# Kernel tuning notes

Hardware: AMD Instinct MI355X
Metric: run time of the kernel (lower is better)

Reference implementation:

```python
import jax, jax.numpy as jnp
import numpy as np

N = 200000   # gaussians
M = 10000    # scaffold nodes
K = 16       # skinning knn
T = 40       # time steps
F = 32       # semantic feature dim
MAX_S = 0.1
MIN_S = 0.0
EPS = 1e-8


def _qnorm(q):
    return q / jnp.clip(jnp.linalg.norm(q, axis=-1, keepdims=True), 1e-12)


def q2R(q):
    # quaternion (w, x, y, z) -> rotation matrix, normalizing first (matches q2R in source)
    q = _qnorm(q)
    w, x, y, z = q[..., 0], q[..., 1], q[..., 2], q[..., 3]
    r0 = jnp.stack([1 - 2 * (y * y + z * z), 2 * (x * y - w * z), 2 * (x * z + w * y)], -1)
    r1 = jnp.stack([2 * (x * y + w * z), 1 - 2 * (x * x + z * z), 2 * (y * z - w * x)], -1)
    r2 = jnp.stack([2 * (x * z - w * y), 2 * (y * z + w * x), 1 - 2 * (x * x + y * y)], -1)
    return jnp.stack([r0, r1, r2], -2)


def quat_mul(a, b):
    aw, ax, ay, az = a[..., 0], a[..., 1], a[..., 2], a[..., 3]
    bw, bx, by, bz = b[..., 0], b[..., 1], b[..., 2], b[..., 3]
    return jnp.stack([
        aw * bw - ax * bx - ay * by - az * bz,
        aw * bx + ax * bw + ay * bz - az * by,
        aw * by - ax * bz + ay * bw + az * bx,
        aw * bz + ax * by - ay * bx + az * bw], -1)


def quat_conj(q):
    return q * jnp.array([1.0, -1.0, -1.0, -1.0], q.dtype)


def setup_inputs() -> dict:
    key = jax.random.key(0)
    ks = jax.random.split(key, 13)
    return {
        "gs_xyz": 0.05 * jax.random.normal(ks[0], (N, 3), jnp.float32),
        "gs_rotation": jax.random.normal(ks[1], (N, 4), jnp.float32),
        "gs_scaling": jax.random.normal(ks[2], (N, 3), jnp.float32),
        "gs_opacity": jax.random.normal(ks[3], (N, 1), jnp.float32),
        "feat_dc": jax.random.normal(ks[4], (N, 3), jnp.float32),
        "feat_rest": jax.random.normal(ks[5], (N, 9), jnp.float32),
        "node_xyz": jax.random.normal(ks[6], (T, M, 3), jnp.float32),
        "node_quat": jax.random.normal(ks[7], (T, M, 4), jnp.float32),
        "node_sigma": 0.1 + 0.5 * jax.random.uniform(ks[8], (M, 1), jnp.float32),
        "node_sem": jax.random.normal(ks[9], (M, F), jnp.float32),
        "attach_ind": jax.random.randint(ks[10], (N,), 0, M, jnp.int32),
        "ref_time": jax.random.randint(ks[11], (N,), 0, T, jnp.int32),
        "topo_knn": jax.random.randint(ks[12], (M, K), 0, M, jnp.int32),
        "t": 5,
    }


def reference(gs_xyz, gs_rotation, gs_scaling, gs_opacity, feat_dc, feat_rest,
              node_xyz, node_quat, node_sigma, node_sem,
              attach_ind, ref_time, topo_knn, t):
    # --- per-gaussian activated attributes ---
    s = MIN_S + jax.nn.sigmoid(gs_scaling) * (MAX_S - MIN_S)   # s_act
    o = jax.nn.sigmoid(gs_opacity)                              # o_act
    sph = jnp.concatenate([feat_dc, feat_rest], axis=-1)        # [N, 12], full sph order

    # --- leaf-local -> world at ref time (get_xyz / get_R_mtx) ---
    ref_p_attach = node_xyz[ref_time, attach_ind]               # [N,3] async knn gather
    ref_q_attach = node_quat[ref_time, attach_ind]              # [N,4]
    R_ref_attach = q2R(ref_q_attach)                            # [N,3,3]
    x_world = jnp.einsum('nij,nj->ni', R_ref_attach, gs_xyz) + ref_p_attach
    R_world = jnp.einsum('nij,njk->nik', R_ref_attach, q2R(gs_rotation))

    # --- scf.warp: KNN skinning from per-point ref time to target time t ---
    sk_ind = topo_knn[attach_ind]                               # [N,K] neighbor node ids
    p_ref = node_xyz[ref_time[:, None], sk_ind]                 # [N,K,3]
    q_ref = node_quat[ref_time[:, None], sk_ind]                # [N,K,4]
    p_live = node_xyz[t][sk_ind]                                # [N,K,3]
    q_live = node_quat[t][sk_ind]                               # [N,K,4]
    sigma = node_sigma[sk_ind, 0]                               # [N,K]

    diff = x_world[:, None, :] - p_ref                          # [N,K,3]
    dsq = jnp.sum(diff * diff, axis=-1)                         # [N,K]
    w = jnp.exp(-dsq / (2.0 * sigma * sigma + EPS))             # RBF skinning weights
    w = w / (jnp.sum(w, axis=-1, keepdims=True) + EPS)          # [N,K]

    # per-node relative transform ref -> live
    q_rel = quat_mul(_qnorm(q_live), quat_conj(_qnorm(q_ref)))  # [N,K,4]
    R_rel = q2R(q_rel)                                          # [N,K,3,3]
    mu_k = jnp.einsum('nkij,nkj->nki', R_rel, diff) + p_live    # [N,K,3]
    mu_live = jnp.einsum('nk,nki->ni', w, mu_k)                 # [N,3]

    q_blend = jnp.einsum('nk,nkd->nd', w, q_rel)                # blended quaternion
    fr_live = jnp.einsum('nij,njk->nik', q2R(q_blend), R_world) # [N,3,3]

    sem_live = jnp.einsum('nk,nkf->nf', w, node_sem[sk_ind])    # [N,F]

    return mu_live, fr_live, s, o, sph, sem_live
```

## Files before the change

kernel.cpp:

```cpp
#include <hip/hip_runtime.h>

#define KNN 16
#define FSEM 32
#define LPG 4
#define NXCD 8
#define NSUB 256

__device__ __forceinline__ float sigmoidf_(float x) { return 1.0f / (1.0f + __expf(-x)); }

__device__ __forceinline__ void quat_to_R(float qw, float qx, float qy, float qz, float* R) {
    float d = qw * qw + qx * qx + qy * qy + qz * qz;
    float inv = rsqrtf(fmaxf(d, 1e-24f));
    float w = qw * inv, x = qx * inv, y = qy * inv, z = qz * inv;
    R[0] = 1.f - 2.f * (y * y + z * z); R[1] = 2.f * (x * y - w * z); R[2] = 2.f * (x * z + w * y);
    R[3] = 2.f * (x * y + w * z); R[4] = 1.f - 2.f * (x * x + z * z); R[5] = 2.f * (y * z - w * x);
    R[6] = 2.f * (x * z - w * y); R[7] = 2.f * (y * z + w * x); R[8] = 1.f - 2.f * (x * x + y * y);
}

__global__ void __launch_bounds__(256)
k_pack_hist(const float* __restrict__ node_xyz, const float* __restrict__ node_quat,
            const float* __restrict__ node_sigma,
            const int* __restrict__ attach, const int* __restrict__ rtime,
            float* __restrict__ packed, int* __restrict__ cnt, int* __restrict__ rank,
            int TM, int M, int N, int shift)
{
    int p = blockIdx.x * blockDim.x + threadIdx.x;
    if (p < TM) {
        const int node = p - (p / M) * M;
        const float* x = node_xyz + 3 * (size_t)p;
        float4 a = make_float4(x[0], x[1], x[2], node_sigma[node]);
        float4 q = reinterpret_cast<const float4*>(node_quat)[p];
        float4* dst = reinterpret_cast<float4*>(packed + 8 * (size_t)p);
        dst[0] = a;
        dst[1] = q;
    }
    if (p < N && cnt) {
        const int key = rtime[p] * NSUB + (attach[p] >> shift);
        rank[p] = atomicAdd(&cnt[key], 1);
    }
}

__global__ void __launch_bounds__(256)
k_scan1(int* __restrict__ cnt, int* __restrict__ blk, int B)
{
    __shared__ int sh[256];
    const int i = blockIdx.x * 256 + threadIdx.x;
    int v = (i < B) ? cnt[i] : 0;
    sh[threadIdx.x] = v;
    __syncthreads();
    int acc = v;
#pragma unroll
    for (int off = 1; off < 256; off <<= 1) {
        int u = (threadIdx.x >= off) ? sh[threadIdx.x - off] : 0;
        __syncthreads();
        acc += u;
        sh[threadIdx.x] = acc;
        __syncthreads();
    }
    if (i < B) cnt[i] = acc - v;
    if (threadIdx.x == 255) blk[blockIdx.x] = acc;
}

__global__ void __launch_bounds__(256)
k_scan2(int* __restrict__ blk, int nblk)
{
    __shared__ int sh[256];
    __shared__ int carry_s;
    if (threadIdx.x == 0) carry_s = 0;
    __syncthreads();
    for (int base = 0; base < nblk; base += 256) {
        const int i = base + threadIdx.x;
        int v = (i < nblk) ? blk[i] : 0;
        sh[threadIdx.x] = v;
        __syncthreads();
        int acc = v;
#pragma unroll
        for (int off = 1; off < 256; off <<= 1) {
            int u = (threadIdx.x >= off) ? sh[threadIdx.x - off] : 0;
            __syncthreads();
            acc += u;
            sh[threadIdx.x] = acc;
            __syncthreads();
        }
        const int carry = carry_s;
        if (i < nblk) blk[i] = acc - v + carry;
        __syncthreads();
        if (threadIdx.x == 255) carry_s = carry + acc;
        __syncthreads();
    }
}

__global__ void __launch_bounds__(256)
k_scatter_elem(const int* __restrict__ attach, const int* __restrict__ rtime,
               const float* __restrict__ gs_xyz,
               const int* __restrict__ rank, const int* __restrict__ cnt,
               const int* __restrict__ blk,
               float4* __restrict__ meta,
               const float* __restrict__ gs_scal,
               const float* __restrict__ gs_opa,
               const float* __restrict__ feat_dc,
               const float* __restrict__ feat_rest,
               float* __restrict__ out,
               int N, int shift)
{
    int n = blockIdx.x * blockDim.x + threadIdx.x;
    if (n >= N) return;
    const int a = attach[n], rt = rtime[n];
    const int key = rt * NSUB + (a >> shift);
    const int pos = cnt[key] + blk[key >> 8] + rank[n];
    meta[2 * (size_t)pos]     = make_float4(__int_as_float(n), __int_as_float(a),
                                            __int_as_float(rt), 0.f);
    meta[2 * (size_t)pos + 1] = make_float4(gs_xyz[3 * (size_t)n + 0],
                                            gs_xyz[3 * (size_t)n + 1],
                                            gs_xyz[3 * (size_t)n + 2], 0.f);

    const size_t Ns = (size_t)N, ns = (size_t)n;
    float* os = out + 12 * Ns + 3 * ns;
    os[0] = 0.1f * sigmoidf_(gs_scal[3 * ns + 0]);
    os[1] = 0.1f * sigmoidf_(gs_scal[3 * ns + 1]);
    os[2] = 0.1f * sigmoidf_(gs_scal[3 * ns + 2]);

    out[15 * Ns + ns] = sigmoidf_(gs_opa[ns]);

    float* osph = out + 16 * Ns + 12 * ns;
    float4 v0 = make_float4(feat_dc[3 * ns + 0], feat_dc[3 * ns + 1], feat_dc[3 * ns + 2],
                            feat_rest[9 * ns + 0]);
    float4 v1 = make_float4(feat_rest[9 * ns + 1], feat_rest[9 * ns + 2],
                            feat_rest[9 * ns + 3], feat_rest[9 * ns + 4]);
    float4 v2 = make_float4(feat_rest[9 * ns + 5], feat_rest[9 * ns + 6],
                            feat_rest[9 * ns + 7], feat_rest[9 * ns + 8]);
    reinterpret_cast<float4*>(osph)[0] = v0;
    reinterpret_cast<float4*>(osph)[1] = v1;
    reinterpret_cast<float4*>(osph)[2] = v2;
}

__global__ void __launch_bounds__(256)
k_elem(const float* __restrict__ gs_scal,
       const float* __restrict__ gs_opa,
       const float* __restrict__ feat_dc,
       const float* __restrict__ feat_rest,
       float* __restrict__ out, int N)
{
    const int n = blockIdx.x * blockDim.x + threadIdx.x;
    if (n >= N) return;
    const size_t Ns = (size_t)N, ns = (size_t)n;

    float* os = out + 12 * Ns + 3 * ns;
    os[0] = 0.1f * sigmoidf_(gs_scal[3 * ns + 0]);
    os[1] = 0.1f * sigmoidf_(gs_scal[3 * ns + 1]);
    os[2] = 0.1f * sigmoidf_(gs_scal[3 * ns + 2]);

    out[15 * Ns + ns] = sigmoidf_(gs_opa[ns]);

    float* osph = out + 16 * Ns + 12 * ns;
    float4 v0 = make_float4(feat_dc[3 * ns + 0], feat_dc[3 * ns + 1], feat_dc[3 * ns + 2],
                            feat_rest[9 * ns + 0]);
    float4 v1 = make_float4(feat_rest[9 * ns + 1], feat_rest[9 * ns + 2],
                            feat_rest[9 * ns + 3], feat_rest[9 * ns + 4]);
    float4 v2 = make_float4(feat_rest[9 * ns + 5], feat_rest[9 * ns + 6],
                            feat_rest[9 * ns + 7], feat_rest[9 * ns + 8]);
    reinterpret_cast<float4*>(osph)[0] = v0;
    reinterpret_cast<float4*>(osph)[1] = v1;
    reinterpret_cast<float4*>(osph)[2] = v2;
}

template<bool PACKED, bool SORTED>
__global__ void __launch_bounds__(256)
dynscf_kernel(const float* __restrict__ gs_xyz,
              const float* __restrict__ gs_rot,
              const float* __restrict__ node_xyz,
              const float* __restrict__ node_quat,
              const float* __restrict__ packed,
              const float* __restrict__ node_sigma,
              const float* __restrict__ node_sem,
              const int* __restrict__ attach_ind,
              const int* __restrict__ ref_time,
              const int* __restrict__ topo_knn,
              const int* __restrict__ t_ptr,
              const float4* __restrict__ meta,
              float* __restrict__ out,
              int N, int M)
{
    int bid = blockIdx.x;
    if (SORTED) {
        const int nwg = gridDim.x;
        const int q = nwg / NXCD, r = nwg % NXCD;
        const int xcd = bid % NXCD, idx = bid / NXCD;
        bid = (xcd < r ? xcd * (q + 1) : r * (q + 1) + (xcd - r) * q) + idx;
    }
    const int tid = bid * blockDim.x + threadIdx.x;
    const int g   = tid >> 2;
    const int sub = tid & (LPG - 1);
    if (g >= N) return;

    const int t = t_ptr[0];

    int n, a, rt;
    float gx, gy, gz;
    if (SORTED) {
        const float4 m0 = meta[2 * (size_t)g];
        const float4 m1 = meta[2 * (size_t)g + 1];
        n  = __float_as_int(m0.x);
        a  = __float_as_int(m0.y);
        rt = __float_as_int(m0.z);
        gx = m1.x; gy = m1.y; gz = m1.z;
    } else {
        n  = g;
        a  = attach_ind[n];
        rt = ref_time[n];
        gx = gs_xyz[3 * (size_t)n + 0];
        gy = gs_xyz[3 * (size_t)n + 1];
        gz = gs_xyz[3 * (size_t)n + 2];
    }

    const size_t base_rt = (size_t)rt * (size_t)M;
    const size_t base_t  = (size_t)t  * (size_t)M;

    const int4 kv = reinterpret_cast<const int4*>(topo_knn)[(size_t)a * (KNN / 4) + sub];
    const int js[4] = { kv.x, kv.y, kv.z, kv.w };

    float apx, apy, apz, aqw, aqx, aqy, aqz;
    if (PACKED) {
        const float4* pk = reinterpret_cast<const float4*>(packed + (base_rt + (size_t)a) * 8);
        float4 xz = pk[0], qv = pk[1];
        apx = xz.x; apy = xz.y; apz = xz.z;
        aqw = qv.x; aqx = qv.y; aqy = qv.z; aqz = qv.w;
    } else {
        const float4 qv = *reinterpret_cast<const float4*>(node_quat + (base_rt + (size_t)a) * 4);
        const float* pa = node_xyz + (base_rt + (size_t)a) * 3;
        apx = pa[0]; apy = pa[1]; apz = pa[2];
        aqw = qv.x; aqx = qv.y; aqy = qv.z; aqz = qv.w;
    }
    float Rref[9];
    quat_to_R(aqw, aqx, aqy, aqz, Rref);

    const float xw0 = Rref[0] * gx + Rref[1] * gy + Rref[2] * gz + apx;
    const float xw1 = Rref[3] * gx + Rref[4] * gy + Rref[5] * gz + apy;
    const float xw2 = Rref[6] * gx + Rref[7] * gy + Rref[8] * gz + apz;

    float wsum = 0.f, mu0 = 0.f, mu1 = 0.f, mu2 = 0.f;
    float qb0 = 0.f, qb1 = 0.f, qb2 = 0.f, qb3 = 0.f;
    float wk[4];

#pragma unroll
    for (int k = 0; k < KNN / LPG; k++) {
        const int j = js[k];

        float prx, pry, prz, rw, rx, ry, rz;
        float plx, ply, plz, lw, lx, ly, lz;
        float sg;
        if (PACKED) {
            const float4* pkr = reinterpret_cast<const float4*>(packed + (base_rt + (size_t)j) * 8);
            float4 xr = pkr[0], qr = pkr[1];
            prx = xr.x; pry = xr.y; prz = xr.z; sg = xr.w;
            rw = qr.x; rx = qr.y; ry = qr.z; rz = qr.w;
            const float4* pkl = reinterpret_cast<const float4*>(packed + (base_t + (size_t)j) * 8);
            float4 xl = pkl[0], ql = pkl[1];
            plx = xl.x; ply = xl.y; plz = xl.z;
            lw = ql.x; lx = ql.y; ly = ql.z; lz = ql.w;
        } else {
            const float* pr = node_xyz + (base_rt + (size_t)j) * 3;
            prx = pr[0]; pry = pr[1]; prz = pr[2];
            const float4 qr = *reinterpret_cast<const float4*>(node_quat + (base_rt + (size_t)j) * 4);
            rw = qr.x; rx = qr.y; ry = qr.z; rz = qr.w;
            const float* pl = node_xyz + (base_t + (size_t)j) * 3;
            plx = pl[0]; ply = pl[1]; plz = pl[2];
            const float4 ql = *reinterpret_cast<const float4*>(node_quat + (base_t + (size_t)j) * 4);
            lw = ql.x; lx = ql.y; ly = ql.z; lz = ql.w;
            sg = node_sigma[j];
        }

        const float dx = xw0 - prx;
        const float dy = xw1 - pry;
        const float dz = xw2 - prz;
        const float dsq = dx * dx + dy * dy + dz * dz;

        const float w = __expf(-dsq / (2.f * sg * sg + 1e-8f));
        wk[k] = w;

        {
            float inv = rsqrtf(fmaxf(rw * rw + rx * rx + ry * ry + rz * rz, 1e-24f));
            rw *= inv; rx *= inv; ry *= inv; rz *= inv;
        }
        {
            float inv = rsqrtf(fmaxf(lw * lw + lx * lx + ly * ly + lz * lz, 1e-24f));
            lw *= inv; lx *= inv; ly *= inv; lz *= inv;
        }
        const float qw =  lw * rw + lx * rx + ly * ry + lz * rz;
        const float qx = -lw * rx + lx * rw - ly * rz + lz * ry;
        const float qy = -lw * ry + lx * rz + ly * rw - lz * rx;
        const float qz = -lw * rz - lx * ry + ly * rx + lz * rw;

        float Rr[9];
        quat_to_R(qw, qx, qy, qz, Rr);

        const float m0 = Rr[0] * dx + Rr[1] * dy + Rr[2] * dz + plx;
        const float m1 = Rr[3] * dx + Rr[4] * dy + Rr[5] * dz + ply;
        const float m2 = Rr[6] * dx + Rr[7] * dy + Rr[8] * dz + plz;

        wsum += w;
        mu0 += w * m0; mu1 += w * m1; mu2 += w * m2;
        qb0 += w * qw; qb1 += w * qx; qb2 += w * qy; qb3 += w * qz;
    }

#pragma unroll
    for (int m = 1; m < LPG; m <<= 1) {
        wsum += __shfl_xor(wsum, m);
        mu0  += __shfl_xor(mu0, m);  mu1 += __shfl_xor(mu1, m);  mu2 += __shfl_xor(mu2, m);
        qb0  += __shfl_xor(qb0, m);  qb1 += __shfl_xor(qb1, m);
        qb2  += __shfl_xor(qb2, m);  qb3 += __shfl_xor(qb3, m);
    }

    const float invw = 1.f / (wsum + 1e-8f);
    const size_t Ns = (size_t)N, ns = (size_t)n;

    float sm0 = 0.f, sm1 = 0.f, sm2 = 0.f, sm3 = 0.f;
    float sm4 = 0.f, sm5 = 0.f, sm6 = 0.f, sm7 = 0.f;
    const float4* sem4 = reinterpret_cast<const float4*>(node_sem);
#pragma unroll
    for (int kk = 0; kk < KNN; kk++) {
        const int src = kk >> 2;
        const int idx = kk & 3;
        const int   jk = __shfl(js[idx], src, LPG);
        const float wkk = __shfl(wk[idx], src, LPG);
        const float4 v0 = sem4[(size_t)jk * (FSEM / 4) + sub * 2 + 0];
        const float4 v1 = sem4[(size_t)jk * (FSEM / 4) + sub * 2 + 1];
        sm0 += wkk * v0.x; sm1 += wkk * v0.y; sm2 += wkk * v0.z; sm3 += wkk * v0.w;
        sm4 += wkk * v1.x; sm5 += wkk * v1.y; sm6 += wkk * v1.z; sm7 += wkk * v1.w;
    }

    if (sub == 0) {
        out[3 * ns + 0] = mu0 * invw;
        out[3 * ns + 1] = mu1 * invw;
        out[3 * ns + 2] = mu2 * invw;
    } else if (sub == 1) {
        const float4 qg = *reinterpret_cast<const float4*>(gs_rot + 4 * ns);
        float Rg[9];
        quat_to_R(qg.x, qg.y, qg.z, qg.w, Rg);
        float Rw[9];
#pragma unroll
        for (int i = 0; i < 3; i++)
#pragma unroll
            for (int j = 0; j < 3; j++)
                Rw[3 * i + j] = Rref[3 * i] * Rg[j] + Rref[3 * i + 1] * Rg[3 + j] + Rref[3 * i + 2] * Rg[6 + j];
        float Rb[9];
        quat_to_R(qb0 * invw, qb1 * invw, qb2 * invw, qb3 * invw, Rb);
        float* ofr = out + 3 * Ns + 9 * ns;
#pragma unroll
        for (int i = 0; i < 3; i++)
#pragma unroll
            for (int j = 0; j < 3; j++)
                ofr[3 * i + j] = Rb[3 * i] * Rw[j] + Rb[3 * i + 1] * Rw[3 + j] + Rb[3 * i + 2] * Rw[6 + j];
    }

    float4* osem = reinterpret_cast<float4*>(out + 28 * Ns + FSEM * ns);
    osem[sub * 2 + 0] = make_float4(sm0 * invw, sm1 * invw, sm2 * invw, sm3 * invw);
    osem[sub * 2 + 1] = make_float4(sm4 * invw, sm5 * invw, sm6 * invw, sm7 * invw);
}

extern "C" void kernel_launch(void* const* d_in, const int* in_sizes, int n_in,
                              void* d_out, int out_size, void* d_ws, size_t ws_size,
                              hipStream_t stream)
{
    const float* gs_xyz     = (const float*)d_in[0];
    const float* gs_rot     = (const float*)d_in[1];
    const float* gs_scal    = (const float*)d_in[2];
    const float* gs_opa     = (const float*)d_in[3];
    const float* feat_dc    = (const float*)d_in[4];
    const float* feat_rest  = (const float*)d_in[5];
    const float* node_xyz   = (const float*)d_in[6];
    const float* node_quat  = (const float*)d_in[7];
    const float* node_sigma = (const float*)d_in[8];
    const float* node_sem   = (const float*)d_in[9];
    const int* attach_ind   = (const int*)d_in[10];
    const int* ref_time     = (const int*)d_in[11];
    const int* topo_knn     = (const int*)d_in[12];
    const int* t_ptr        = (const int*)d_in[13];

    const int N = in_sizes[0] / 3;
    const int M = in_sizes[8];
    const int TM = in_sizes[6] / 3;
    const int T  = TM / M;
    const int B  = T * NSUB;

    int shift = 0;
    while (((M - 1) >> shift) >= NSUB) shift++;

    float* out = (float*)d_out;

    const int block = 256;
    const int gridN = (N + block - 1) / block;
    const long long threads = (long long)N * LPG;
    const int gridM = (int)((threads + block - 1) / block);
    const int gridPH = (((TM > N ? TM : N)) + block - 1) / block;
    const int nblkS = (B + 255) / 256;

    const size_t f_packed = (size_t)TM * 8;
    const size_t f_meta   = (size_t)N * 8;
    const size_t i_cnt    = (size_t)B;
    const size_t i_blk    = (size_t)nblkS;
    const size_t i_rank   = (size_t)N;
    const size_t need_sort   = (f_packed + f_meta + i_cnt + i_blk + i_rank) * sizeof(float);
    const size_t need_packed = f_packed * sizeof(float);

    if (ws_size >= need_sort) {
        float*  packed = (float*)d_ws;
        float4* meta   = (float4*)(packed + f_packed);
        int*    cnt    = (int*)(packed + f_packed + f_meta);
        int*    blk    = cnt + i_cnt;
        int*    rank   = blk + i_blk;

        hipMemsetAsync(cnt, 0, (size_t)B * sizeof(int), stream);
        hipLaunchKernelGGL(k_pack_hist, dim3(gridPH), dim3(block), 0, stream,
                           node_xyz, node_quat, node_sigma, attach_ind, ref_time,
                           packed, cnt, rank, TM, M, N, shift);
        hipLaunchKernelGGL(k_scan1, dim3(nblkS), dim3(block), 0, stream, cnt, blk, B);
        hipLaunchKernelGGL(k_scan2, dim3(1), dim3(block), 0, stream, blk, nblkS);
        hipLaunchKernelGGL(k_scatter_elem, dim3(gridN), dim3(block), 0, stream,
                           attach_ind, ref_time, gs_xyz, rank, cnt, blk, meta,
                           gs_scal, gs_opa, feat_dc, feat_rest, out, N, shift);
        hipLaunchKernelGGL((dynscf_kernel<true, true>), dim3(gridM), dim3(block), 0, stream,
                           gs_xyz, gs_rot, node_xyz, node_quat, packed, node_sigma, node_sem,
                           attach_ind, ref_time, topo_knn, t_ptr, meta, out, N, M);
    } else if (ws_size >= need_packed) {
        float* packed = (float*)d_ws;
        hipLaunchKernelGGL(k_pack_hist, dim3(gridPH), dim3(block), 0, stream,
                           node_xyz, node_quat, node_sigma, attach_ind, ref_time,
                           packed, (int*)nullptr, (int*)nullptr, TM, M, 0, shift);
        hipLaunchKernelGGL((dynscf_kernel<true, false>), dim3(gridM), dim3(block), 0, stream,
                           gs_xyz, gs_rot, node_xyz, node_quat, packed, node_sigma, node_sem,
                           attach_ind, ref_time, topo_knn, t_ptr, (const float4*)nullptr,
                           out, N, M);
        hipLaunchKernelGGL(k_elem, dim3(gridN), dim3(block), 0, stream,
                           gs_scal, gs_opa, feat_dc, feat_rest, out, N);
    } else {
        hipLaunchKernelGGL((dynscf_kernel<false, false>), dim3(gridM), dim3(block), 0, stream,
                           gs_xyz, gs_rot, node_xyz, node_quat, (const float*)nullptr,
                           node_sigma, node_sem,
                           attach_ind, ref_time, topo_knn, t_ptr, (const float4*)nullptr,
                           out, N, M);
        hipLaunchKernelGGL(k_elem, dim3(gridN), dim3(block), 0, stream,
                           gs_scal, gs_opa, feat_dc, feat_rest, out, N);
    }
}
```

Baseline: 216.3 us.

## Replace two-level counting sort with per-timestep block-aggregated bucket sort

Drops the fine key (ref_time × attach bucket) counting sort and its two scan kernels. Instead it bins only by ref_time, using shared-memory histograms with one global atomic per block per timestep, and computes each block's offset with a serial prefix over T. It also packs the gaussian rotation into the sorted meta record so the main kernel reads it contiguously, and moves the reference rotation matrix into the sub==1 lane to shorten live ranges. The aim is fewer launches and less contention on global atomics. The cost is coarser sorting: elements are no longer grouped by attach node, so gather locality within a timestep may drop, and the meta record grows by one float4 per gaussian.

```diff
diff --git a/kernel.cpp b/kernel.cpp
--- a/kernel.cpp
+++ b/kernel.cpp
@@ -4,7 +4,8 @@
 #define FSEM 32
 #define LPG 4
 #define NXCD 8
-#define NSUB 256
+#define CSTRIDE 32
+#define MAXT 256
 
 __device__ __forceinline__ float sigmoidf_(float x) { return 1.0f / (1.0f + __expf(-x)); }
 
@@ -20,11 +21,17 @@
 __global__ void __launch_bounds__(256)
 k_pack_hist(const float* __restrict__ node_xyz, const float* __restrict__ node_quat,
             const float* __restrict__ node_sigma,
-            const int* __restrict__ attach, const int* __restrict__ rtime,
-            float* __restrict__ packed, int* __restrict__ cnt, int* __restrict__ rank,
-            int TM, int M, int N, int shift)
+            const int* __restrict__ rtime,
+            float* __restrict__ packed, int* __restrict__ cnt,
+            int TM, int M, int N, int T)
 {
-    int p = blockIdx.x * blockDim.x + threadIdx.x;
+    __shared__ int lh[MAXT];
+    if (threadIdx.x < MAXT) lh[threadIdx.x] = 0;
+    __syncthreads();
+
+    const int p = blockIdx.x * blockDim.x + threadIdx.x;
+    if (cnt && p < N) atomicAdd(&lh[rtime[p]], 1);
+
     if (p < TM) {
         const int node = p - (p / M) * M;
         const float* x = node_xyz + 3 * (size_t)p;
@@ -34,85 +41,66 @@
         dst[0] = a;
         dst[1] = q;
     }
-    if (p < N && cnt) {
-        const int key = rtime[p] * NSUB + (attach[p] >> shift);
-        rank[p] = atomicAdd(&cnt[key], 1);
-    }
-}
-
-__global__ void __launch_bounds__(256)
-k_scan1(int* __restrict__ cnt, int* __restrict__ blk, int B)
-{
-    __shared__ int sh[256];
-    const int i = blockIdx.x * 256 + threadIdx.x;
-    int v = (i < B) ? cnt[i] : 0;
-    sh[threadIdx.x] = v;
-    __syncthreads();
-    int acc = v;
-#pragma unroll
-    for (int off = 1; off < 256; off <<= 1) {
-        int u = (threadIdx.x >= off) ? sh[threadIdx.x - off] : 0;
-        __syncthreads();
-        acc += u;
-        sh[threadIdx.x] = acc;
-        __syncthreads();
-    }
-    if (i < B) cnt[i] = acc - v;
-    if (threadIdx.x == 255) blk[blockIdx.x] = acc;
-}
-
-__global__ void __launch_bounds__(256)
-k_scan2(int* __restrict__ blk, int nblk)
-{
-    __shared__ int sh[256];
-    __shared__ int carry_s;
-    if (threadIdx.x == 0) carry_s = 0;
-    __syncthreads();
-    for (int base = 0; base < nblk; base += 256) {
-        const int i = base + threadIdx.x;
-        int v = (i < nblk) ? blk[i] : 0;
-        sh[threadIdx.x] = v;
-        __syncthreads();
-        int acc = v;
-#pragma unroll
-        for (int off = 1; off < 256; off <<= 1) {
-            int u = (threadIdx.x >= off) ? sh[threadIdx.x - off] : 0;
-            __syncthreads();
-            acc += u;
-            sh[threadIdx.x] = acc;
-            __syncthreads();
-        }
-        const int carry = carry_s;
-        if (i < nblk) blk[i] = acc - v + carry;
-        __syncthreads();
-        if (threadIdx.x == 255) carry_s = carry + acc;
-        __syncthreads();
+
+    __syncthreads();
+    if (cnt && threadIdx.x < T) {
+        const int c = lh[threadIdx.x];
+        if (c > 0) atomicAdd(&cnt[threadIdx.x * CSTRIDE], c);
     }
 }
 
 __global__ void __launch_bounds__(256)
 k_scatter_elem(const int* __restrict__ attach, const int* __restrict__ rtime,
                const float* __restrict__ gs_xyz,
-               const int* __restrict__ rank, const int* __restrict__ cnt,
-               const int* __restrict__ blk,
+               const float* __restrict__ gs_rot,
+               const int* __restrict__ cnt, int* __restrict__ cur,
                float4* __restrict__ meta,
                const float* __restrict__ gs_scal,
                const float* __restrict__ gs_opa,
                const float* __restrict__ feat_dc,
                const float* __restrict__ feat_rest,
                float* __restrict__ out,
-               int N, int shift)
+               int N, int T)
 {
-    int n = blockIdx.x * blockDim.x + threadIdx.x;
-    if (n >= N) return;
-    const int a = attach[n], rt = rtime[n];
-    const int key = rt * NSUB + (a >> shift);
-    const int pos = cnt[key] + blk[key >> 8] + rank[n];
-    meta[2 * (size_t)pos]     = make_float4(__int_as_float(n), __int_as_float(a),
-                                            __int_as_float(rt), 0.f);
-    meta[2 * (size_t)pos + 1] = make_float4(gs_xyz[3 * (size_t)n + 0],
+    __shared__ int lh[MAXT];
+    __shared__ int bb[MAXT];
+    __shared__ int pref[MAXT];
+
+    if (threadIdx.x < MAXT) lh[threadIdx.x] = 0;
+    __syncthreads();
+
+    const int n = blockIdx.x * blockDim.x + threadIdx.x;
+    const bool valid = (n < N);
+    int a = 0, rt = 0, lrank = 0;
+    if (valid) {
+        a  = attach[n];
+        rt = rtime[n];
+        lrank = atomicAdd(&lh[rt], 1);
+    }
+    __syncthreads();
+
+    if (threadIdx.x < T) {
+        const int c = lh[threadIdx.x];
+        bb[threadIdx.x] = (c > 0) ? atomicAdd(&cur[threadIdx.x * CSTRIDE], c) : 0;
+        pref[threadIdx.x] = cnt[threadIdx.x * CSTRIDE];
+    }
+    __syncthreads();
+    if (threadIdx.x == 0) {
+        int run = 0;
+#pragma unroll 4
+        for (int i = 0; i < T; i++) { const int c = pref[i]; pref[i] = run; run += c; }
+    }
+    __syncthreads();
+
+    if (!valid) return;
+
+    const int pos = pref[rt] + bb[rt] + lrank;
+    meta[3 * (size_t)pos]     = make_float4(__int_as_float(n), 0.f,
+                                            __int_as_float(rt), __int_as_float(a));
+    meta[3 * (size_t)pos + 1] = make_float4(gs_xyz[3 * (size_t)n + 0],
                                             gs_xyz[3 * (size_t)n + 1],
                                             gs_xyz[3 * (size_t)n + 2], 0.f);
+    meta[3 * (size_t)pos + 2] = reinterpret_cast<const float4*>(gs_rot)[n];
 
     const size_t Ns = (size_t)N, ns = (size_t)n;
     float* os = out + 12 * Ns + 3 * ns;
@@ -198,11 +186,11 @@
     int n, a, rt;
     float gx, gy, gz;
     if (SORTED) {
-        const float4 m0 = meta[2 * (size_t)g];
-        const float4 m1 = meta[2 * (size_t)g + 1];
+        const float4 m0 = meta[3 * (size_t)g];
+        const float4 m1 = meta[3 * (size_t)g + 1];
         n  = __float_as_int(m0.x);
-        a  = __float_as_int(m0.y);
         rt = __float_as_int(m0.z);
+        a  = __float_as_int(m0.w);
         gx = m1.x; gy = m1.y; gz = m1.z;
     } else {
         n  = g;
@@ -231,12 +219,14 @@
         apx = pa[0]; apy = pa[1]; apz = pa[2];
         aqw = qv.x; aqx = qv.y; aqy = qv.z; aqz = qv.w;
     }
-    float Rref[9];
-    quat_to_R(aqw, aqx, aqy, aqz, Rref);
-
-    const float xw0 = Rref[0] * gx + Rref[1] * gy + Rref[2] * gz + apx;
-    const float xw1 = Rref[3] * gx + Rref[4] * gy + Rref[5] * gz + apy;
-    const float xw2 = Rref[6] * gx + Rref[7] * gy + Rref[8] * gz + apz;
+    float xw0, xw1, xw2;
+    {
+        float Rf[9];
+        quat_to_R(aqw, aqx, aqy, aqz, Rf);
+        xw0 = Rf[0] * gx + Rf[1] * gy + Rf[2] * gz + apx;
+        xw1 = Rf[3] * gx + Rf[4] * gy + Rf[5] * gz + apy;
+        xw2 = Rf[6] * gx + Rf[7] * gy + Rf[8] * gz + apz;
+    }
 
     float wsum = 0.f, mu0 = 0.f, mu1 = 0.f, mu2 = 0.f;
     float qb0 = 0.f, qb1 = 0.f, qb2 = 0.f, qb3 = 0.f;
@@ -334,7 +324,11 @@
         out[3 * ns + 1] = mu1 * invw;
         out[3 * ns + 2] = mu2 * invw;
     } else if (sub == 1) {
-        const float4 qg = *reinterpret_cast<const float4*>(gs_rot + 4 * ns);
+        float4 qg;
+        if (SORTED) qg = meta[3 * (size_t)g + 2];
+        else        qg = *reinterpret_cast<const float4*>(gs_rot + 4 * ns);
+        float Rref[9];
+        quat_to_R(aqw, aqx, aqy, aqz, Rref);
         float Rg[9];
         quat_to_R(qg.x, qg.y, qg.z, qg.w, Rg);
         float Rw[9];
@@ -381,10 +375,6 @@
     const int M = in_sizes[8];
     const int TM = in_sizes[6] / 3;
     const int T  = TM / M;
-    const int B  = T * NSUB;
-
-    int shift = 0;
-    while (((M - 1) >> shift) >= NSUB) shift++;
 
     float* out = (float*)d_out;
 
@@ -393,40 +383,35 @@
     const long long threads = (long long)N * LPG;
     const int gridM = (int)((threads + block - 1) / block);
     const int gridPH = (((TM > N ? TM : N)) + block - 1) / block;
-    const int nblkS = (B + 255) / 256;
 
     const size_t f_packed = (size_t)TM * 8;
-    const size_t f_meta   = (size_t)N * 8;
-    const size_t i_cnt    = (size_t)B;
-    const size_t i_blk    = (size_t)nblkS;
-    const size_t i_rank   = (size_t)N;
-    const size_t need_sort   = (f_packed + f_meta + i_cnt + i_blk + i_rank) * sizeof(float);
+    const size_t f_meta   = (size_t)N * 12;
+    const size_t i_cnt    = (size_t)MAXT * CSTRIDE;
+    const size_t i_cur    = (size_t)MAXT * CSTRIDE;
+    const size_t need_sort   = (f_packed + f_meta + i_cnt + i_cur) * sizeof(float);
     const size_t need_packed = f_packed * sizeof(float);
 
-    if (ws_size >= need_sort) {
+    if (ws_size >= need_sort && T <= MAXT) {
         float*  packed = (float*)d_ws;
         float4* meta   = (float4*)(packed + f_packed);
         int*    cnt    = (int*)(packed + f_packed + f_meta);
-        int*    blk    = cnt + i_cnt;
-        int*    rank   = blk + i_blk;
-
-        hipMemsetAsync(cnt, 0, (size_t)B * sizeof(int), stream);
+        int*    cur    = cnt + i_cnt;
+
+        hipMemsetAsync(cnt, 0, (i_cnt + i_cur) * sizeof(int), stream);
         hipLaunchKernelGGL(k_pack_hist, dim3(gridPH), dim3(block), 0, stream,
-                           node_xyz, node_quat, node_sigma, attach_ind, ref_time,
-                           packed, cnt, rank, TM, M, N, shift);
-        hipLaunchKernelGGL(k_scan1, dim3(nblkS), dim3(block), 0, stream, cnt, blk, B);
-        hipLaunchKernelGGL(k_scan2, dim3(1), dim3(block), 0, stream, blk, nblkS);
+                           node_xyz, node_quat, node_sigma, ref_time,
+                           packed, cnt, TM, M, N, T);
         hipLaunchKernelGGL(k_scatter_elem, dim3(gridN), dim3(block), 0, stream,
-                           attach_ind, ref_time, gs_xyz, rank, cnt, blk, meta,
-                           gs_scal, gs_opa, feat_dc, feat_rest, out, N, shift);
+                           attach_ind, ref_time, gs_xyz, gs_rot, cnt, cur, meta,
+                           gs_scal, gs_opa, feat_dc, feat_rest, out, N, T);
         hipLaunchKernelGGL((dynscf_kernel<true, true>), dim3(gridM), dim3(block), 0, stream,
                            gs_xyz, gs_rot, node_xyz, node_quat, packed, node_sigma, node_sem,
                            attach_ind, ref_time, topo_knn, t_ptr, meta, out, N, M);
     } else if (ws_size >= need_packed) {
         float* packed = (float*)d_ws;
         hipLaunchKernelGGL(k_pack_hist, dim3(gridPH), dim3(block), 0, stream,
-                           node_xyz, node_quat, node_sigma, attach_ind, ref_time,
-                           packed, (int*)nullptr, (int*)nullptr, TM, M, 0, shift);
+                           node_xyz, node_quat, node_sigma, ref_time,
+                           packed, (int*)nullptr, TM, M, 0, T);
         hipLaunchKernelGGL((dynscf_kernel<true, false>), dim3(gridM), dim3(block), 0, stream,
                            gs_xyz, gs_rot, node_xyz, node_quat, packed, node_sigma, node_sem,
                            attach_ind, ref_time, topo_knn, t_ptr, (const float4*)nullptr,
```

Result: no change. 212.2 us (-1.9%).

## Sort gaussians by exact (time,node) key, prenormalize node quats, gather rotations

Applied to the files above, without the earlier changes.

Replaces the coarse 256-bucket sort with a full counting sort keyed on (ref_time, attach node), so the rank array goes away and positions come from atomics during the scatter. Node quaternions are normalized once in the pack kernel, which removes the per-neighbor rsqrt work in the main kernel. Gaussian rotations are also scattered into sorted order so the main kernel reads them contiguously. The costs are a larger histogram and scan (T*M entries instead of T*256), more bytes written during the scatter, and within-bucket order that now depends on atomic ordering.

```diff
diff --git a/kernel.cpp b/kernel.cpp
--- a/kernel.cpp
+++ b/kernel.cpp
@@ -4,7 +4,6 @@
 #define FSEM 32
 #define LPG 4
 #define NXCD 8
-#define NSUB 256
 
 __device__ __forceinline__ float sigmoidf_(float x) { return 1.0f / (1.0f + __expf(-x)); }
 
@@ -17,26 +16,54 @@
     R[6] = 2.f * (x * z - w * y); R[7] = 2.f * (y * z + w * x); R[8] = 1.f - 2.f * (x * x + y * y);
 }
 
+__device__ __forceinline__ void elem_outputs(int n, int N,
+                                             const float* __restrict__ gs_scal,
+                                             const float* __restrict__ gs_opa,
+                                             const float* __restrict__ feat_dc,
+                                             const float* __restrict__ feat_rest,
+                                             float* __restrict__ out)
+{
+    const size_t Ns = (size_t)N, ns = (size_t)n;
+    float* os = out + 12 * Ns + 3 * ns;
+    os[0] = 0.1f * sigmoidf_(gs_scal[3 * ns + 0]);
+    os[1] = 0.1f * sigmoidf_(gs_scal[3 * ns + 1]);
+    os[2] = 0.1f * sigmoidf_(gs_scal[3 * ns + 2]);
+
+    out[15 * Ns + ns] = sigmoidf_(gs_opa[ns]);
+
+    float* osph = out + 16 * Ns + 12 * ns;
+    float4 v0 = make_float4(feat_dc[3 * ns + 0], feat_dc[3 * ns + 1], feat_dc[3 * ns + 2],
+                            feat_rest[9 * ns + 0]);
+    float4 v1 = make_float4(feat_rest[9 * ns + 1], feat_rest[9 * ns + 2],
+                            feat_rest[9 * ns + 3], feat_rest[9 * ns + 4]);
+    float4 v2 = make_float4(feat_rest[9 * ns + 5], feat_rest[9 * ns + 6],
+                            feat_rest[9 * ns + 7], feat_rest[9 * ns + 8]);
+    reinterpret_cast<float4*>(osph)[0] = v0;
+    reinterpret_cast<float4*>(osph)[1] = v1;
+    reinterpret_cast<float4*>(osph)[2] = v2;
+}
+
 __global__ void __launch_bounds__(256)
 k_pack_hist(const float* __restrict__ node_xyz, const float* __restrict__ node_quat,
             const float* __restrict__ node_sigma,
             const int* __restrict__ attach, const int* __restrict__ rtime,
-            float* __restrict__ packed, int* __restrict__ cnt, int* __restrict__ rank,
-            int TM, int M, int N, int shift)
-{
-    int p = blockIdx.x * blockDim.x + threadIdx.x;
+            float* __restrict__ packed, int* __restrict__ cnt,
+            int TM, int M, int N)
+{
+    const int p = blockIdx.x * blockDim.x + threadIdx.x;
     if (p < TM) {
         const int node = p - (p / M) * M;
         const float* x = node_xyz + 3 * (size_t)p;
+        float4 q = reinterpret_cast<const float4*>(node_quat)[p];
+        const float inv = rsqrtf(fmaxf(q.x * q.x + q.y * q.y + q.z * q.z + q.w * q.w, 1e-24f));
+        q.x *= inv; q.y *= inv; q.z *= inv; q.w *= inv;
         float4 a = make_float4(x[0], x[1], x[2], node_sigma[node]);
-        float4 q = reinterpret_cast<const float4*>(node_quat)[p];
         float4* dst = reinterpret_cast<float4*>(packed + 8 * (size_t)p);
         dst[0] = a;
         dst[1] = q;
     }
-    if (p < N && cnt) {
-        const int key = rtime[p] * NSUB + (attach[p] >> shift);
-        rank[p] = atomicAdd(&cnt[key], 1);
+    if (cnt && p < N) {
+        atomicAdd(&cnt[rtime[p] * M + attach[p]], 1);
     }
 }
 
@@ -93,45 +120,30 @@
 __global__ void __launch_bounds__(256)
 k_scatter_elem(const int* __restrict__ attach, const int* __restrict__ rtime,
                const float* __restrict__ gs_xyz,
-               const int* __restrict__ rank, const int* __restrict__ cnt,
-               const int* __restrict__ blk,
-               float4* __restrict__ meta,
+               const float* __restrict__ gs_rot,
+               int* __restrict__ cnt, const int* __restrict__ blk,
+               float4* __restrict__ metaA, float4* __restrict__ rotA,
                const float* __restrict__ gs_scal,
                const float* __restrict__ gs_opa,
                const float* __restrict__ feat_dc,
                const float* __restrict__ feat_rest,
                float* __restrict__ out,
-               int N, int shift)
-{
-    int n = blockIdx.x * blockDim.x + threadIdx.x;
+               int N, int M)
+{
+    const int n = blockIdx.x * blockDim.x + threadIdx.x;
     if (n >= N) return;
     const int a = attach[n], rt = rtime[n];
-    const int key = rt * NSUB + (a >> shift);
-    const int pos = cnt[key] + blk[key >> 8] + rank[n];
-    meta[2 * (size_t)pos]     = make_float4(__int_as_float(n), __int_as_float(a),
-                                            __int_as_float(rt), 0.f);
-    meta[2 * (size_t)pos + 1] = make_float4(gs_xyz[3 * (size_t)n + 0],
-                                            gs_xyz[3 * (size_t)n + 1],
-                                            gs_xyz[3 * (size_t)n + 2], 0.f);
-
-    const size_t Ns = (size_t)N, ns = (size_t)n;
-    float* os = out + 12 * Ns + 3 * ns;
-    os[0] = 0.1f * sigmoidf_(gs_scal[3 * ns + 0]);
-    os[1] = 0.1f * sigmoidf_(gs_scal[3 * ns + 1]);
-    os[2] = 0.1f * sigmoidf_(gs_scal[3 * ns + 2]);
-
-    out[15 * Ns + ns] = sigmoidf_(gs_opa[ns]);
-
-    float* osph = out + 16 * Ns + 12 * ns;
-    float4 v0 = make_float4(feat_dc[3 * ns + 0], feat_dc[3 * ns + 1], feat_dc[3 * ns + 2],
-                            feat_rest[9 * ns + 0]);
-    float4 v1 = make_float4(feat_rest[9 * ns + 1], feat_rest[9 * ns + 2],
-                            feat_rest[9 * ns + 3], feat_rest[9 * ns + 4]);
-    float4 v2 = make_float4(feat_rest[9 * ns + 5], feat_rest[9 * ns + 6],
-                            feat_rest[9 * ns + 7], feat_rest[9 * ns + 8]);
-    reinterpret_cast<float4*>(osph)[0] = v0;
-    reinterpret_cast<float4*>(osph)[1] = v1;
-    reinterpret_cast<float4*>(osph)[2] = v2;
+    const int key = rt * M + a;
+    const int pos = blk[key >> 8] + atomicAdd(&cnt[key], 1);
+
+    metaA[2 * (size_t)pos]     = make_float4(__int_as_float(n), __int_as_float(a),
+                                             __int_as_float(rt), 0.f);
+    metaA[2 * (size_t)pos + 1] = make_float4(gs_xyz[3 * (size_t)n + 0],
+                                             gs_xyz[3 * (size_t)n + 1],
+                                             gs_xyz[3 * (size_t)n + 2], 0.f);
+    rotA[pos] = reinterpret_cast<const float4*>(gs_rot)[n];
+
+    elem_outputs(n, N, gs_scal, gs_opa, feat_dc, feat_rest, out);
 }
 
 __global__ void __launch_bounds__(256)
@@ -143,25 +155,7 @@
 {
     const int n = blockIdx.x * blockDim.x + threadIdx.x;
     if (n >= N) return;
-    const size_t Ns = (size_t)N, ns = (size_t)n;
-
-    float* os = out + 12 * Ns + 3 * ns;
-    os[0] = 0.1f * sigmoidf_(gs_scal[3 * ns + 0]);
-    os[1] = 0.1f * sigmoidf_(gs_scal[3 * ns + 1]);
-    os[2] = 0.1f * sigmoidf_(gs_scal[3 * ns + 2]);
-
-    out[15 * Ns + ns] = sigmoidf_(gs_opa[ns]);
-
-    float* osph = out + 16 * Ns + 12 * ns;
-    float4 v0 = make_float4(feat_dc[3 * ns + 0], feat_dc[3 * ns + 1], feat_dc[3 * ns + 2],
-                            feat_rest[9 * ns + 0]);
-    float4 v1 = make_float4(feat_rest[9 * ns + 1], feat_rest[9 * ns + 2],
-                            feat_rest[9 * ns + 3], feat_rest[9 * ns + 4]);
-    float4 v2 = make_float4(feat_rest[9 * ns + 5], feat_rest[9 * ns + 6],
-                            feat_rest[9 * ns + 7], feat_rest[9 * ns + 8]);
-    reinterpret_cast<float4*>(osph)[0] = v0;
-    reinterpret_cast<float4*>(osph)[1] = v1;
-    reinterpret_cast<float4*>(osph)[2] = v2;
+    elem_outputs(n, N, gs_scal, gs_opa, feat_dc, feat_rest, out);
 }
 
 template<bool PACKED, bool SORTED>
@@ -177,7 +171,8 @@
               const int* __restrict__ ref_time,
               const int* __restrict__ topo_knn,
               const int* __restrict__ t_ptr,
-              const float4* __restrict__ meta,
+              const float4* __restrict__ metaA,
+              const float4* __restrict__ rotA,
               float* __restrict__ out,
               int N, int M)
 {
@@ -198,8 +193,8 @@
     int n, a, rt;
     float gx, gy, gz;
     if (SORTED) {
-        const float4 m0 = meta[2 * (size_t)g];
-        const float4 m1 = meta[2 * (size_t)g + 1];
+        const float4 m0 = metaA[2 * (size_t)g];
+        const float4 m1 = metaA[2 * (size_t)g + 1];
         n  = __float_as_int(m0.x);
         a  = __float_as_int(m0.y);
         rt = __float_as_int(m0.z);
@@ -231,12 +226,14 @@
         apx = pa[0]; apy = pa[1]; apz = pa[2];
         aqw = qv.x; aqx = qv.y; aqy = qv.z; aqz = qv.w;
     }
-    float Rref[9];
-    quat_to_R(aqw, aqx, aqy, aqz, Rref);
-
-    const float xw0 = Rref[0] * gx + Rref[1] * gy + Rref[2] * gz + apx;
-    const float xw1 = Rref[3] * gx + Rref[4] * gy + Rref[5] * gz + apy;
-    const float xw2 = Rref[6] * gx + Rref[7] * gy + Rref[8] * gz + apz;
+    float xw0, xw1, xw2;
+    {
+        float Rf[9];
+        quat_to_R(aqw, aqx, aqy, aqz, Rf);
+        xw0 = Rf[0] * gx + Rf[1] * gy + Rf[2] * gz + apx;
+        xw1 = Rf[3] * gx + Rf[4] * gy + Rf[5] * gz + apy;
+        xw2 = Rf[6] * gx + Rf[7] * gy + Rf[8] * gz + apz;
+    }
 
     float wsum = 0.f, mu0 = 0.f, mu1 = 0.f, mu2 = 0.f;
     float qb0 = 0.f, qb1 = 0.f, qb2 = 0.f, qb3 = 0.f;
@@ -278,12 +275,10 @@
         const float w = __expf(-dsq / (2.f * sg * sg + 1e-8f));
         wk[k] = w;
 
-        {
+        if (!PACKED) {
             float inv = rsqrtf(fmaxf(rw * rw + rx * rx + ry * ry + rz * rz, 1e-24f));
             rw *= inv; rx *= inv; ry *= inv; rz *= inv;
-        }
-        {
-            float inv = rsqrtf(fmaxf(lw * lw + lx * lx + ly * ly + lz * lz, 1e-24f));
+            inv = rsqrtf(fmaxf(lw * lw + lx * lx + ly * ly + lz * lz, 1e-24f));
             lw *= inv; lx *= inv; ly *= inv; lz *= inv;
         }
         const float qw =  lw * rw + lx * rx + ly * ry + lz * rz;
@@ -334,7 +329,11 @@
         out[3 * ns + 1] = mu1 * invw;
         out[3 * ns + 2] = mu2 * invw;
     } else if (sub == 1) {
-        const float4 qg = *reinterpret_cast<const float4*>(gs_rot + 4 * ns);
+        float4 qg;
+        if (SORTED) qg = rotA[g];
+        else        qg = *reinterpret_cast<const float4*>(gs_rot + 4 * ns);
+        float Rref[9];
+        quat_to_R(aqw, aqx, aqy, aqz, Rref);
         float Rg[9];
         quat_to_R(qg.x, qg.y, qg.z, qg.w, Rg);
         float Rw[9];
@@ -380,11 +379,8 @@
     const int N = in_sizes[0] / 3;
     const int M = in_sizes[8];
     const int TM = in_sizes[6] / 3;
-    const int T  = TM / M;
-    const int B  = T * NSUB;
-
-    int shift = 0;
-    while (((M - 1) >> shift) >= NSUB) shift++;
+    const int B  = TM;
+    const int nchunk = (B + 255) / 256;
 
     float* out = (float*)d_out;
 
@@ -393,52 +389,52 @@
     const long long threads = (long long)N * LPG;
     const int gridM = (int)((threads + block - 1) / block);
     const int gridPH = (((TM > N ? TM : N)) + block - 1) / block;
-    const int nblkS = (B + 255) / 256;
 
     const size_t f_packed = (size_t)TM * 8;
     const size_t f_meta   = (size_t)N * 8;
+    const size_t f_rot    = (size_t)N * 4;
     const size_t i_cnt    = (size_t)B;
-    const size_t i_blk    = (size_t)nblkS;
-    const size_t i_rank   = (size_t)N;
-    const size_t need_sort   = (f_packed + f_meta + i_cnt + i_blk + i_rank) * sizeof(float);
+    const size_t i_blk    = 4096;
+    const size_t need_sort   = (f_packed + f_meta + f_rot + i_cnt + i_blk) * sizeof(float);
     const size_t need_packed = f_packed * sizeof(float);
 
-    if (ws_size >= need_sort) {
+    if (ws_size >= need_sort && nchunk <= 4096) {
         float*  packed = (float*)d_ws;
-        float4* meta   = (float4*)(packed + f_packed);
-        int*    cnt    = (int*)(packed + f_packed + f_meta);
+        float4* metaA  = (float4*)(packed + f_packed);
+        float4* rotA   = (float4*)(packed + f_packed + f_meta);
+        int*    cnt    = (int*)(packed + f_packed + f_meta + f_rot);
         int*    blk    = cnt + i_cnt;
-        int*    rank   = blk + i_blk;
 
         hipMemsetAsync(cnt, 0, (size_t)B * sizeof(int), stream);
         hipLaunchKernelGGL(k_pack_hist, dim3(gridPH), dim3(block), 0, stream,
                            node_xyz, node_quat, node_sigma, attach_ind, ref_time,
-                           packed, cnt, rank, TM, M, N, shift);
-        hipLaunchKernelGGL(k_scan1, dim3(nblkS), dim3(block), 0, stream, cnt, blk, B);
-        hipLaunchKernelGGL(k_scan2, dim3(1), dim3(block), 0, stream, blk, nblkS);
+                           packed, cnt, TM, M, N);
+        hipLaunchKernelGGL(k_scan1, dim3(nchunk), dim3(block), 0, stream, cnt, blk, B);
+        hipLaunchKernelGGL(k_scan2, dim3(1), dim3(block), 0, stream, blk, nchunk);
         hipLaunchKernelGGL(k_scatter_elem, dim3(gridN), dim3(block), 0, stream,
-                           attach_ind, ref_time, gs_xyz, rank, cnt, blk, meta,
-                           gs_scal, gs_opa, feat_dc, feat_rest, out, N, shift);
+                           attach_ind, ref_time, gs_xyz, gs_rot, cnt, blk,
+                           metaA, rotA, gs_scal, gs_opa, feat_dc, feat_rest,
+                           out, N, M);
         hipLaunchKernelGGL((dynscf_kernel<true, true>), dim3(gridM), dim3(block), 0, stream,
                            gs_xyz, gs_rot, node_xyz, node_quat, packed, node_sigma, node_sem,
-                           attach_ind, ref_time, topo_knn, t_ptr, meta, out, N, M);
+                           attach_ind, ref_time, topo_knn, t_ptr, metaA, rotA, out, N, M);
     } else if (ws_size >= need_packed) {
         float* packed = (float*)d_ws;
         hipLaunchKernelGGL(k_pack_hist, dim3(gridPH), dim3(block), 0, stream,
                            node_xyz, node_quat, node_sigma, attach_ind, ref_time,
-                           packed, (int*)nullptr, (int*)nullptr, TM, M, 0, shift);
+                           packed, (int*)nullptr, TM, M, 0);
         hipLaunchKernelGGL((dynscf_kernel<true, false>), dim3(gridM), dim3(block), 0, stream,
                            gs_xyz, gs_rot, node_xyz, node_quat, packed, node_sigma, node_sem,
-                           attach_ind, ref_time, topo_knn, t_ptr, (const float4*)nullptr,
-                           out, N, M);
+                           attach_ind, ref_time, topo_knn, t_ptr,
+                           (const float4*)nullptr, (const float4*)nullptr, out, N, M);
         hipLaunchKernelGGL(k_elem, dim3(gridN), dim3(block), 0, stream,
                            gs_scal, gs_opa, feat_dc, feat_rest, out, N);
     } else {
         hipLaunchKernelGGL((dynscf_kernel<false, false>), dim3(gridM), dim3(block), 0, stream,
                            gs_xyz, gs_rot, node_xyz, node_quat, (const float*)nullptr,
                            node_sigma, node_sem,
-                           attach_ind, ref_time, topo_knn, t_ptr, (const float4*)nullptr,
-                           out, N, M);
+                           attach_ind, ref_time, topo_knn, t_ptr,
+                           (const float4*)nullptr, (const float4*)nullptr, out, N, M);
         hipLaunchKernelGGL(k_elem, dim3(gridN), dim3(block), 0, stream,
                            gs_scal, gs_opa, feat_dc, feat_rest, out, N);
     }
```

After: 214.8 us. No clear change (-0.7%).
